# Kernel tuning notes

Hardware: AMD Instinct MI355X
Metric: run time of the kernel (lower is better)

## Reference

```python
import jax, jax.numpy as jnp
import numpy as np

B, Q, S, H = 2048, 128, 128, 32  # batch, num slices, slice length, hidden dim
C = Q * S


def setup_inputs() -> dict:
    key = jax.random.key(0)
    k0, k1, k2 = jax.random.split(key, 3)
    x = jax.random.normal(k0, (B, 1, 1, C), dtype=jnp.float32)
    # stacked per-slice MLP params (Glorot-ish scaling)
    W1 = jax.random.normal(k1, (Q, S, H), dtype=jnp.float32) * (1.0 / np.sqrt(S))
    b1 = jnp.zeros((Q, H), dtype=jnp.float32)
    W2 = jax.random.normal(k2, (Q, H, 1), dtype=jnp.float32) * (1.0 / np.sqrt(H))
    b2 = jnp.zeros((Q, 1), dtype=jnp.float32)
    return {"x": x, "W1": W1, "b1": b1, "W2": W2, "b2": b2}


def reference(x, W1, b1, W2, b2):
    # (B,1,1,C) -> (B,Q,S): slice the channel dim into Q groups
    xs = x.reshape(x.shape[0], Q, -1)
    # per-slice Dense(H) with ELU: grouped GEMM over the Q axis
    h = jax.nn.elu(jnp.einsum("bqs,qsh->bqh", xs, W1) + b1)  # (B,Q,H)
    # per-slice Dense(1): contract hidden dim -> scalar per slice
    out = jnp.einsum("bqh,qh->bq", h, W2[..., 0]) + b2[..., 0]  # (B,Q)
    return out
```

## Files before the change

kernel.cpp:

```cpp
#include <hip/hip_runtime.h>
#include <hip/hip_bf16.h>
#include <math.h>

#define QN 128
#define SN 128
#define HN 32
#define CN (QN * SN)
#define TILE_R 128

using half8   = __attribute__((ext_vector_type(8))) _Float16;
using floatx4 = __attribute__((ext_vector_type(4))) float;

__global__ __launch_bounds__(256, 4)
void divenc_kernel(const float* __restrict__ x,
                   const float* __restrict__ W1,
                   const float* __restrict__ b1,
                   const float* __restrict__ W2,
                   const float* __restrict__ b2,
                   float* __restrict__ out) {
  const int q    = blockIdx.x;
  const int b0   = blockIdx.y * TILE_R;
  const int tid  = threadIdx.x;
  const int lane = tid & 63;
  const int wid  = __builtin_amdgcn_readfirstlane(tid >> 6);
  const int nA   = lane & 15;
  const int koct = lane >> 4;

  const float* __restrict__ w1q = W1 + (size_t)q * (SN * HN);
  half8 bf[2][4];
  #pragma unroll
  for (int n0 = 0; n0 < 2; ++n0) {
    #pragma unroll
    for (int kk = 0; kk < 4; ++kk) {
      #pragma unroll
      for (int i = 0; i < 8; ++i) {
        const int k = kk * 32 + koct * 8 + i;
        bf[n0][kk][i] = (_Float16)w1q[k * HN + n0 * 16 + nA];
      }
    }
  }

  floatx4 z = {0.f, 0.f, 0.f, 0.f};
  floatx4 acc[2][2];
  acc[0][0] = z; acc[0][1] = z; acc[1][0] = z; acc[1][1] = z;

  const int row0 = b0 + wid * 32;
  #pragma unroll
  for (int mt = 0; mt < 2; ++mt) {
    const float* __restrict__ rp =
        x + (size_t)(row0 + mt * 16 + nA) * CN + q * SN + koct * 8;
    #pragma unroll
    for (int kk = 0; kk < 4; ++kk) {
      const float4 va = *reinterpret_cast<const float4*>(rp + kk * 32);
      const float4 vb = *reinterpret_cast<const float4*>(rp + kk * 32 + 4);
      half8 af;
      af[0] = (_Float16)va.x; af[1] = (_Float16)va.y;
      af[2] = (_Float16)va.z; af[3] = (_Float16)va.w;
      af[4] = (_Float16)vb.x; af[5] = (_Float16)vb.y;
      af[6] = (_Float16)vb.z; af[7] = (_Float16)vb.w;
      acc[mt][0] = __builtin_amdgcn_mfma_f32_16x16x32_f16(af, bf[0][kk], acc[mt][0], 0, 0, 0);
      acc[mt][1] = __builtin_amdgcn_mfma_f32_16x16x32_f16(af, bf[1][kk], acc[mt][1], 0, 0, 0);
    }
  }

  const float b1a = b1[q * HN + nA],  b1b = b1[q * HN + 16 + nA];
  const float w2a = W2[q * HN + nA],  w2b = W2[q * HN + 16 + nA];
  const float b2q = b2[q];

  #pragma unroll
  for (int mt = 0; mt < 2; ++mt) {
    #pragma unroll
    for (int reg = 0; reg < 4; ++reg) {
      float v0 = acc[mt][0][reg] + b1a;
      v0 = v0 > 0.f ? v0 : expm1f(v0);
      float v1 = acc[mt][1][reg] + b1b;
      v1 = v1 > 0.f ? v1 : expm1f(v1);
      float t = fmaf(v0, w2a, v1 * w2b);
      t += __shfl_xor(t, 1);
      t += __shfl_xor(t, 2);
      t += __shfl_xor(t, 4);
      t += __shfl_xor(t, 8);
      if (nA == 0) {
        const int row = row0 + mt * 16 + koct * 4 + reg;
        out[(size_t)row * QN + q] = t + b2q;
      }
    }
  }
}

extern "C" void kernel_launch(void* const* d_in, const int* in_sizes, int n_in,
                              void* d_out, int out_size, void* d_ws, size_t ws_size,
                              hipStream_t stream) {
  const float* x  = (const float*)d_in[0];
  const float* W1 = (const float*)d_in[1];
  const float* b1 = (const float*)d_in[2];
  const float* W2 = (const float*)d_in[3];
  const float* b2 = (const float*)d_in[4];
  float* out = (float*)d_out;

  const int B = in_sizes[0] / CN;
  dim3 grid(QN, B / TILE_R);
  divenc_kernel<<<grid, 256, 0, stream>>>(x, W1, b1, W2, b2, out);
}
```

Before: 29.92 us.

## Stage x tile into LDS via global_load_lds with XOR swizzle

Replaces the per-lane strided float4 global loads of x with direct global-to-LDS async loads, where each row's 512-byte slice is fetched contiguously. The tile is stored in a 64KB shared buffer with an XOR swizzle so the later MFMA operand reads avoid bank conflicts. Bias and W2 loads move ahead of the barrier to overlap with the transfer. The large LDS footprint and launch bounds lowered to 2 blocks per SM reduce occupancy, and a block-wide sync is added.

```diff
diff --git a/kernel.cpp b/kernel.cpp
--- a/kernel.cpp
+++ b/kernel.cpp
@@ -8,10 +8,18 @@
 #define CN (QN * SN)
 #define TILE_R 128
 
+typedef unsigned int u32;
 using half8   = __attribute__((ext_vector_type(8))) _Float16;
 using floatx4 = __attribute__((ext_vector_type(4))) float;
 
-__global__ __launch_bounds__(256, 4)
+__device__ __forceinline__ void gload16(const float* g, float* l) {
+  __builtin_amdgcn_global_load_lds(
+      (const __attribute__((address_space(1))) u32*)(const void*)g,
+      (__attribute__((address_space(3))) u32*)(void*)l,
+      16, 0, 0);
+}
+
+__global__ __launch_bounds__(256, 2)
 void divenc_kernel(const float* __restrict__ x,
                    const float* __restrict__ W1,
                    const float* __restrict__ b1,
@@ -26,6 +34,21 @@
   const int nA   = lane & 15;
   const int koct = lane >> 4;
 
+  __shared__ float xs[TILE_R * SN];
+
+  {
+    const float* tb = x + (size_t)b0 * CN + (size_t)q * SN;
+    const int rl = lane >> 5;
+    const int s  = lane & 31;
+    #pragma unroll
+    for (int k = 0; k < 16; ++k) {
+      const int rloc = wid * 32 + k * 2 + rl;
+      const int g    = s ^ (rloc & 15);
+      gload16(tb + (size_t)rloc * CN + g * 4,
+              xs + wid * 4096 + k * 256);
+    }
+  }
+
   const float* __restrict__ w1q = W1 + (size_t)q * (SN * HN);
   half8 bf[2][4];
   #pragma unroll
@@ -39,20 +62,27 @@
       }
     }
   }
+  const float b1a = b1[q * HN + nA],  b1b = b1[q * HN + 16 + nA];
+  const float w2a = W2[q * HN + nA],  w2b = W2[q * HN + 16 + nA];
+  const float b2q = b2[q];
 
-  floatx4 z = {0.f, 0.f, 0.f, 0.f};
+  __syncthreads();
+
+  const floatx4 z = {0.f, 0.f, 0.f, 0.f};
   floatx4 acc[2][2];
   acc[0][0] = z; acc[0][1] = z; acc[1][0] = z; acc[1][1] = z;
 
-  const int row0 = b0 + wid * 32;
   #pragma unroll
   for (int mt = 0; mt < 2; ++mt) {
-    const float* __restrict__ rp =
-        x + (size_t)(row0 + mt * 16 + nA) * CN + q * SN + koct * 8;
+    const int row = wid * 32 + mt * 16 + nA;
+    const float* rowbase = xs + row * SN;
     #pragma unroll
     for (int kk = 0; kk < 4; ++kk) {
-      const float4 va = *reinterpret_cast<const float4*>(rp + kk * 32);
-      const float4 vb = *reinterpret_cast<const float4*>(rp + kk * 32 + 4);
+      const int g0 = kk * 8 + koct * 2;
+      const float4 va = *reinterpret_cast<const float4*>(
+          rowbase + ((g0 ^ nA) << 2));
+      const float4 vb = *reinterpret_cast<const float4*>(
+          rowbase + (((g0 + 1) ^ nA) << 2));
       half8 af;
       af[0] = (_Float16)va.x; af[1] = (_Float16)va.y;
       af[2] = (_Float16)va.z; af[3] = (_Float16)va.w;
@@ -62,10 +92,6 @@
       acc[mt][1] = __builtin_amdgcn_mfma_f32_16x16x32_f16(af, bf[1][kk], acc[mt][1], 0, 0, 0);
     }
   }
-
-  const float b1a = b1[q * HN + nA],  b1b = b1[q * HN + 16 + nA];
-  const float w2a = W2[q * HN + nA],  w2b = W2[q * HN + 16 + nA];
-  const float b2q = b2[q];
 
   #pragma unroll
   for (int mt = 0; mt < 2; ++mt) {
@@ -81,7 +107,7 @@
       t += __shfl_xor(t, 4);
       t += __shfl_xor(t, 8);
       if (nA == 0) {
-        const int row = row0 + mt * 16 + koct * 4 + reg;
+        const int row = b0 + wid * 32 + mt * 16 + koct * 4 + reg;
         out[(size_t)row * QN + q] = t + b2q;
       }
     }
```

Measured after the change: 35.80 us. 19.6% more time.
